# Performance work log

Measured on AMD Instinct MI355X. Metric: run time of the kernel, lower is better.

## Reference

```python
import jax, jax.numpy as jnp
import numpy as np

B, S, D_IN, D_OUT = 4, 2048, 1024, 1024


def setup_inputs() -> dict:
    key = jax.random.key(0)
    ks = jax.random.split(key, 7)
    s_in = 1.0 / np.sqrt(D_IN)
    return {
        "x": jax.random.normal(ks[0], (B, S, D_IN), dtype=jnp.float32),
        "Wq": jax.random.uniform(ks[1], (D_IN, D_OUT), jnp.float32, -s_in, s_in),
        "bq": jax.random.uniform(ks[2], (D_OUT,), jnp.float32, -s_in, s_in),
        "Wk": jax.random.uniform(ks[3], (D_IN, D_OUT), jnp.float32, -s_in, s_in),
        "bk": jax.random.uniform(ks[4], (D_OUT,), jnp.float32, -s_in, s_in),
        "Wv": jax.random.uniform(ks[5], (D_IN, D_OUT), jnp.float32, -s_in, s_in),
        "bv": jax.random.uniform(ks[6], (D_OUT,), jnp.float32, -s_in, s_in),
    }


def reference(x, Wq, bq, Wk, bk, Wv, bv):
    # Linear projections (torch Linear: x @ W^T + b; here W stored as [in,out])
    q = x @ Wq + bq  # [B,S,D]
    k = x @ Wk + bk
    v = x @ Wv + bv
    scores = jnp.einsum("bqd,bkd->bqk", q, k)  # [B,S,S]
    # causal mask: positions j > i masked with -inf (applied BEFORE scaling,
    # which is equivalent since -inf/sqrt(d) == -inf)
    seq = scores.shape[-1]
    causal = jnp.tril(jnp.ones((seq, seq), dtype=bool))
    masked = jnp.where(causal, scores, -jnp.inf)
    attn = jax.nn.softmax(masked / np.sqrt(k.shape[-1]), axis=-1)
    # dropout p=0.0 -> identity
    return attn @ v  # [B,S,D]
```

## Files before the change

kernel.cpp:

```cpp
#include <hip/hip_runtime.h>

typedef unsigned short u16;
typedef unsigned int u32;
typedef __attribute__((ext_vector_type(8))) short short8;
typedef __attribute__((ext_vector_type(4))) float f32x4;

__device__ __forceinline__ u16 f2bf(float f) {
    u32 u = __float_as_uint(f);
    u32 r = (u + 0x7fffu + ((u >> 16) & 1u)) >> 16;
    return (u16)r;
}
__device__ __forceinline__ float bf2f(u16 h) {
    return __uint_as_float(((u32)h) << 16);
}

__device__ __forceinline__ void gld16(u16* lds_dst, const u16* g_src) {
    __builtin_amdgcn_global_load_lds(
        (const __attribute__((address_space(1))) unsigned int*)g_src,
        (__attribute__((address_space(3))) unsigned int*)lds_dst,
        16, 0, 0);
}

__global__ void split_x_k(const float* __restrict__ x, u16* __restrict__ xh,
                          u16* __restrict__ xl) {
    long i = ((long)blockIdx.x * 256 + threadIdx.x) * 4;
    float4 f = *(const float4*)(x + i);
    u16 h0 = f2bf(f.x), h1 = f2bf(f.y), h2 = f2bf(f.z), h3 = f2bf(f.w);
    u16 l0 = f2bf(f.x - bf2f(h0)), l1 = f2bf(f.y - bf2f(h1));
    u16 l2 = f2bf(f.z - bf2f(h2)), l3 = f2bf(f.w - bf2f(h3));
    uint2 hv, lv;
    hv.x = (u32)h0 | ((u32)h1 << 16); hv.y = (u32)h2 | ((u32)h3 << 16);
    lv.x = (u32)l0 | ((u32)l1 << 16); lv.y = (u32)l2 | ((u32)l3 << 16);
    *(uint2*)(xh + i) = hv;
    *(uint2*)(xl + i) = lv;
}

__global__ void splitT_w_k(const float* __restrict__ Wq, const float* __restrict__ Wk,
                           const float* __restrict__ Wv, u16* __restrict__ wth,
                           u16* __restrict__ wtl) {
    __shared__ float tile[32][33];
    int z = blockIdx.z;
    const float* W = (z == 0) ? Wq : (z == 1) ? Wk : Wv;
    int n0 = blockIdx.x * 32, k0 = blockIdx.y * 32;
    int tx = threadIdx.x, ty = threadIdx.y;
#pragma unroll
    for (int r0 = 0; r0 < 4; ++r0) {
        int r = ty + r0 * 8;
        tile[r][tx] = W[(long)(k0 + r) * 1024 + n0 + tx];
    }
    __syncthreads();
    long zoff = (long)z * 1024 * 1024;
#pragma unroll
    for (int r0 = 0; r0 < 4; ++r0) {
        int r = ty + r0 * 8;
        float f = tile[tx][r];
        u16 h = f2bf(f), l = f2bf(f - bf2f(h));
        long idx = zoff + (long)(n0 + r) * 1024 + k0 + tx;
        wth[idx] = h;
        wtl[idx] = l;
    }
}

__global__ void transpose_v_k(const u16* __restrict__ vh, const u16* __restrict__ vl,
                              u16* __restrict__ vth, u16* __restrict__ vtl) {
    __shared__ u16 th[32][33];
    __shared__ u16 tl[32][33];
    int z = blockIdx.z;
    int d0 = blockIdx.x * 32, s0 = blockIdx.y * 32;
    int tx = threadIdx.x, ty = threadIdx.y;
#pragma unroll
    for (int r0 = 0; r0 < 4; ++r0) {
        int r = ty + r0 * 8;
        long idx = ((long)z * 2048 + s0 + r) * 1024 + d0 + tx;
        th[r][tx] = vh[idx];
        tl[r][tx] = vl[idx];
    }
    __syncthreads();
    long zoff = (long)z * 1024 * 2048;
#pragma unroll
    for (int r0 = 0; r0 < 4; ++r0) {
        int r = ty + r0 * 8;
        long idx = zoff + (long)(d0 + r) * 2048 + s0 + tx;
        vth[idx] = th[tx][r];
        vtl[idx] = tl[tx][r];
    }
}

template <int MODE>
__launch_bounds__(256, 2)
__global__ void gemm_k(const u16* __restrict__ Ah, const u16* __restrict__ Al, long sAz,
                       const u16* __restrict__ Bh, const u16* __restrict__ Bl, long sBz,
                       int lda, int ldb, int Ksize,
                       float* __restrict__ outF, long sCz, int ldc,
                       u16* __restrict__ oh0, u16* __restrict__ oh1, u16* __restrict__ oh2,
                       u16* __restrict__ ol0, u16* __restrict__ ol1, u16* __restrict__ ol2,
                       const float* __restrict__ b0, const float* __restrict__ b1,
                       const float* __restrict__ b2) {
    const int bi = blockIdx.x, bj = blockIdx.y, z = blockIdx.z;
    if (MODE == 1 && bj > bi) return;

    int ksteps = Ksize / 32;
    if (MODE == 2) ksteps = min(ksteps, (bi + 1) * 4);

    Ah += (long)z * sAz; Al += (long)z * sAz;
    Bh += (long)z * sBz; Bl += (long)z * sBz;

    __shared__ u16 lds[4 * 4096];
    u16* tAh = lds;
    u16* tAl = lds + 4096;
    u16* tBh = lds + 8192;
    u16* tBl = lds + 12288;

    const int t = threadIdx.x;
    const int lane = t & 63, w = t >> 6;
    const int wr = w >> 1, wc = w & 1;

    f32x4 acc[4][4] = {};

    const int srow = (lane >> 2);
    const int scol = (lane & 3) * 8;
    const long rowA = (long)bi * 128;
    const long rowB = (long)bj * 128;

    for (int ks = 0; ks < ksteps; ++ks) {
        const int k0 = ks * 32;
#pragma unroll
        for (int i = 0; i < 2; ++i) {
            const int chunk = i * 4 + w;
            const int r = chunk * 16 + srow;
            const long aoff = (rowA + r) * (long)lda + k0 + scol;
            const long boff = (rowB + r) * (long)ldb + k0 + scol;
            gld16(tAh + chunk * 512, Ah + aoff);
            gld16(tAl + chunk * 512, Al + aoff);
            gld16(tBh + chunk * 512, Bh + boff);
            gld16(tBl + chunk * 512, Bl + boff);
        }
        __syncthreads();

        short8 afh[4], afl[4], bfh[4], bfl[4];
        const int fr = lane & 15;
        const int koff = (lane >> 4) * 8;
#pragma unroll
        for (int m = 0; m < 4; ++m) {
            int r = wr * 64 + m * 16 + fr;
            afh[m] = *(const short8*)&tAh[r * 32 + koff];
            afl[m] = *(const short8*)&tAl[r * 32 + koff];
        }
#pragma unroll
        for (int n = 0; n < 4; ++n) {
            int r = wc * 64 + n * 16 + fr;
            bfh[n] = *(const short8*)&tBh[r * 32 + koff];
            bfl[n] = *(const short8*)&tBl[r * 32 + koff];
        }
#pragma unroll
        for (int m = 0; m < 4; ++m)
#pragma unroll
            for (int n = 0; n < 4; ++n) {
                acc[m][n] = __builtin_amdgcn_mfma_f32_16x16x32_bf16(afh[m], bfh[n], acc[m][n], 0, 0, 0);
                acc[m][n] = __builtin_amdgcn_mfma_f32_16x16x32_bf16(afh[m], bfl[n], acc[m][n], 0, 0, 0);
                acc[m][n] = __builtin_amdgcn_mfma_f32_16x16x32_bf16(afl[m], bfh[n], acc[m][n], 0, 0, 0);
            }
        __syncthreads();
    }

    const int row0 = bi * 128 + wr * 64 + (lane >> 4) * 4;
    const int col0 = bj * 128 + wc * 64 + (lane & 15);

    if (MODE == 0) {
        const float* bias = (z == 0) ? b0 : (z == 1) ? b1 : b2;
        u16* oh = (z == 0) ? oh0 : (z == 1) ? oh1 : oh2;
        u16* ol = (z == 0) ? ol0 : (z == 1) ? ol1 : ol2;
#pragma unroll
        for (int n = 0; n < 4; ++n) {
            float bv = bias[col0 + n * 16];
#pragma unroll
            for (int m = 0; m < 4; ++m)
#pragma unroll
                for (int j = 0; j < 4; ++j) {
                    float v = acc[m][n][j] + bv;
                    long idx = (long)(row0 + m * 16 + j) * ldc + col0 + n * 16;
                    u16 h = f2bf(v);
                    oh[idx] = h;
                    ol[idx] = f2bf(v - bf2f(h));
                }
        }
    } else {
        float* o = outF + (long)z * sCz;
#pragma unroll
        for (int m = 0; m < 4; ++m)
#pragma unroll
            for (int n = 0; n < 4; ++n)
#pragma unroll
                for (int j = 0; j < 4; ++j)
                    o[(long)(row0 + m * 16 + j) * ldc + col0 + n * 16] = acc[m][n][j];
    }
}

__global__ void softmax_k(const float* __restrict__ S, u16* __restrict__ Ph,
                          u16* __restrict__ Pl) {
    const long row = blockIdx.x;
    const int batch = (int)(row >> 11), i = (int)(row & 2047);
    const float* srow = S + ((long)batch * 2048 + i) * 2048;
    u16* ph = Ph + row * 2048;
    u16* pl = Pl + row * 2048;
    const int t = threadIdx.x;

    float v[8];
    float m = -1e30f;
#pragma unroll
    for (int j = 0; j < 8; ++j) {
        int c = j * 256 + t;
        float x = (c <= i) ? srow[c] : -1e30f;
        v[j] = x;
        m = fmaxf(m, x);
    }
#pragma unroll
    for (int off = 32; off; off >>= 1) m = fmaxf(m, __shfl_xor(m, off));
    __shared__ float redm[4], reds[4];
    if ((t & 63) == 0) redm[t >> 6] = m;
    __syncthreads();
    m = fmaxf(fmaxf(redm[0], redm[1]), fmaxf(redm[2], redm[3]));

    float p[8];
    float s = 0.f;
#pragma unroll
    for (int j = 0; j < 8; ++j) {
        int c = j * 256 + t;
        float e = (c <= i) ? __expf((v[j] - m) * 0.03125f) : 0.f;
        p[j] = e;
        s += e;
    }
#pragma unroll
    for (int off = 32; off; off >>= 1) s += __shfl_xor(s, off);
    if ((t & 63) == 0) reds[t >> 6] = s;
    __syncthreads();
    s = reds[0] + reds[1] + reds[2] + reds[3];
    const float inv = 1.f / s;
#pragma unroll
    for (int j = 0; j < 8; ++j) {
        int c = j * 256 + t;
        float o = p[j] * inv;
        u16 h = f2bf(o);
        ph[c] = h;
        pl[c] = f2bf(o - bf2f(h));
    }
}

extern "C" void kernel_launch(void* const* d_in, const int* in_sizes, int n_in,
                              void* d_out, int out_size, void* d_ws, size_t ws_size,
                              hipStream_t stream) {
    const float* x  = (const float*)d_in[0];
    const float* Wq = (const float*)d_in[1];
    const float* bq = (const float*)d_in[2];
    const float* Wk = (const float*)d_in[3];
    const float* bk = (const float*)d_in[4];
    const float* Wv = (const float*)d_in[5];
    const float* bv = (const float*)d_in[6];
    float* out = (float*)d_out;
    char* ws = (char*)d_ws;
    const size_t MB = 1ull << 20;

    u16* xs_hi = (u16*)(ws + 0 * MB);
    u16* xs_lo = (u16*)(ws + 16 * MB);
    u16* wt_hi = (u16*)(ws + 32 * MB);
    u16* wt_lo = (u16*)(ws + 38 * MB);
    float* S   = (float*)(ws + 0 * MB);
    u16* q_hi = (u16*)(ws + 64 * MB);
    u16* q_lo = (u16*)(ws + 80 * MB);
    u16* k_hi = (u16*)(ws + 96 * MB);
    u16* k_lo = (u16*)(ws + 112 * MB);
    u16* P_hi = (u16*)(ws + 64 * MB);
    u16* P_lo = (u16*)(ws + 96 * MB);
    u16* v_hi  = (u16*)(ws + 128 * MB);
    u16* v_lo  = (u16*)(ws + 144 * MB);
    u16* vt_hi = (u16*)(ws + 160 * MB);
    u16* vt_lo = (u16*)(ws + 176 * MB);

    split_x_k<<<8192, 256, 0, stream>>>(x, xs_hi, xs_lo);
    splitT_w_k<<<dim3(32, 32, 3), dim3(32, 8), 0, stream>>>(Wq, Wk, Wv, wt_hi, wt_lo);
    gemm_k<0><<<dim3(64, 8, 3), 256, 0, stream>>>(
        xs_hi, xs_lo, 0L, wt_hi, wt_lo, 1024L * 1024, 1024, 1024, 1024,
        nullptr, 0L, 1024, q_hi, k_hi, v_hi, q_lo, k_lo, v_lo, bq, bk, bv);
    transpose_v_k<<<dim3(32, 64, 4), dim3(32, 8), 0, stream>>>(v_hi, v_lo, vt_hi, vt_lo);
    gemm_k<1><<<dim3(16, 16, 4), 256, 0, stream>>>(
        q_hi, q_lo, 2048L * 1024, k_hi, k_lo, 2048L * 1024, 1024, 1024, 1024,
        S, 2048L * 2048, 2048, nullptr, nullptr, nullptr, nullptr, nullptr, nullptr,
        nullptr, nullptr, nullptr);
    softmax_k<<<8192, 256, 0, stream>>>(S, P_hi, P_lo);
    gemm_k<2><<<dim3(16, 8, 4), 256, 0, stream>>>(
        P_hi, P_lo, 2048L * 2048, vt_hi, vt_lo, 1024L * 2048, 2048, 2048, 2048,
        out, 2048L * 1024, 1024, nullptr, nullptr, nullptr, nullptr, nullptr, nullptr,
        nullptr, nullptr, nullptr);
}
```

Before: 473.1 us.

## Triple-buffer GEMM LDS loads with swizzle, 512-thread blocks, trim softmax stores

Restructures the split-bf16 GEMM into a 3-slot LDS ring. Global-to-LDS loads for step h+2 are issued while step h computes, using explicit vmcnt waits and a single barrier per step in place of two syncthreads. Blocks go to 512 threads (8 waves), tile width becomes a template parameter (256 columns for the projection GEMM, 128 for the others), LDS accesses get an XOR swizzle to avoid bank conflicts, and MFMA sections run under raised wave priority. Softmax now skips writing P entries beyond the 128-aligned causal limit that the PV GEMM never reads. In exchange, LDS use per block grows and hand-tuned waitcnt counts tie correctness to the exact number of loads issued per stage.

Measured after the change: 468.4 us. No clear change (-1.0%).

```diff
diff --git a/kernel.cpp b/kernel.cpp
--- a/kernel.cpp
+++ b/kernel.cpp
@@ -86,8 +86,8 @@
     }
 }
 
-template <int MODE>
-__launch_bounds__(256, 2)
+template <int MODE, int NF>
+__launch_bounds__(512, 2)
 __global__ void gemm_k(const u16* __restrict__ Ah, const u16* __restrict__ Al, long sAz,
                        const u16* __restrict__ Bh, const u16* __restrict__ Bl, long sBz,
                        int lda, int ldb, int Ksize,
@@ -96,82 +96,103 @@
                        u16* __restrict__ ol0, u16* __restrict__ ol1, u16* __restrict__ ol2,
                        const float* __restrict__ b0, const float* __restrict__ b1,
                        const float* __restrict__ b2) {
+    constexpr int BN = NF * 64;
+    constexpr int SLOT = 8192 + NF * 4096;
+    __shared__ u16 lds[3 * SLOT];
+
     const int bi = blockIdx.x, bj = blockIdx.y, z = blockIdx.z;
     if (MODE == 1 && bj > bi) return;
-
-    int ksteps = Ksize / 32;
-    if (MODE == 2) ksteps = min(ksteps, (bi + 1) * 4);
-
-    Ah += (long)z * sAz; Al += (long)z * sAz;
-    Bh += (long)z * sBz; Bl += (long)z * sBz;
-
-    __shared__ u16 lds[4 * 4096];
-    u16* tAh = lds;
-    u16* tAl = lds + 4096;
-    u16* tBh = lds + 8192;
-    u16* tBl = lds + 12288;
-
-    const int t = threadIdx.x;
-    const int lane = t & 63, w = t >> 6;
-    const int wr = w >> 1, wc = w & 1;
-
-    f32x4 acc[4][4] = {};
-
-    const int srow = (lane >> 2);
-    const int scol = (lane & 3) * 8;
-    const long rowA = (long)bi * 128;
-    const long rowB = (long)bj * 128;
-
-    for (int ks = 0; ks < ksteps; ++ks) {
-        const int k0 = ks * 32;
-#pragma unroll
-        for (int i = 0; i < 2; ++i) {
-            const int chunk = i * 4 + w;
-            const int r = chunk * 16 + srow;
-            const long aoff = (rowA + r) * (long)lda + k0 + scol;
-            const long boff = (rowB + r) * (long)ldb + k0 + scol;
-            gld16(tAh + chunk * 512, Ah + aoff);
-            gld16(tAl + chunk * 512, Al + aoff);
-            gld16(tBh + chunk * 512, Bh + boff);
-            gld16(tBl + chunk * 512, Bl + boff);
-        }
-        __syncthreads();
-
-        short8 afh[4], afl[4], bfh[4], bfl[4];
-        const int fr = lane & 15;
-        const int koff = (lane >> 4) * 8;
+    int nsteps = Ksize / 32;
+    if (MODE == 2) nsteps = min(nsteps, (bi + 1) * 4);
+
+    const u16* gA_h = Ah + (long)z * sAz;
+    const u16* gA_l = Al + (long)z * sAz;
+    const u16* gB_h = Bh + (long)z * sBz;
+    const u16* gB_l = Bl + (long)z * sBz;
+
+    const int tid = threadIdx.x;
+    const int lane = tid & 63, w = tid >> 6;
+    const int wr = w >> 2, wc = w & 3;
+
+    const int srow = tid >> 2;
+    const int ls8 = (((tid & 3) ^ ((tid >> 3) & 3)) << 3);
+    const long aoff  = ((long)bi * 128 + srow) * lda + ls8;
+    const long boff0 = ((long)bj * BN + srow) * ldb + ls8;
+    const long boff1 = boff0 + 128L * (long)ldb;
+    const int wbase = w * 512;
+
+    f32x4 acc[4][NF] = {};
+
+    const int fr = lane & 15;
+    const int ps8 = (((lane >> 4) ^ ((fr >> 1) & 3)) << 3);
+
+    auto stage = [&](int slot, int step) {
+        const int k0 = step * 32;
+        u16* sb = lds + slot * SLOT;
+        gld16(sb + wbase,              gA_h + aoff + k0);
+        gld16(sb + 4096 + wbase,       gA_l + aoff + k0);
+        gld16(sb + 8192 + wbase,       gB_h + boff0 + k0);
+        if constexpr (NF == 4) gld16(sb + 12288 + wbase, gB_h + boff1 + k0);
+        gld16(sb + 8192 + NF * 2048 + wbase, gB_l + boff0 + k0);
+        if constexpr (NF == 4) gld16(sb + 8192 + NF * 2048 + 4096 + wbase, gB_l + boff1 + k0);
+    };
+
+    auto compute = [&](int slot) {
+        const u16* LA = lds + slot * SLOT;
+        const u16* LB = LA + 8192;
+        short8 afh[4], afl[4], bfh[NF], bfl[NF];
 #pragma unroll
         for (int m = 0; m < 4; ++m) {
-            int r = wr * 64 + m * 16 + fr;
-            afh[m] = *(const short8*)&tAh[r * 32 + koff];
-            afl[m] = *(const short8*)&tAl[r * 32 + koff];
-        }
-#pragma unroll
-        for (int n = 0; n < 4; ++n) {
-            int r = wc * 64 + n * 16 + fr;
-            bfh[n] = *(const short8*)&tBh[r * 32 + koff];
-            bfl[n] = *(const short8*)&tBl[r * 32 + koff];
-        }
+            int off = (wr * 64 + m * 16 + fr) * 32 + ps8;
+            afh[m] = *(const short8*)(LA + off);
+            afl[m] = *(const short8*)(LA + 4096 + off);
+        }
+#pragma unroll
+        for (int n = 0; n < NF; ++n) {
+            int off = (wc * (NF * 16) + n * 16 + fr) * 32 + ps8;
+            bfh[n] = *(const short8*)(LB + off);
+            bfl[n] = *(const short8*)(LB + NF * 2048 + off);
+        }
+        __builtin_amdgcn_s_setprio(1);
 #pragma unroll
         for (int m = 0; m < 4; ++m)
 #pragma unroll
-            for (int n = 0; n < 4; ++n) {
+            for (int n = 0; n < NF; ++n) {
                 acc[m][n] = __builtin_amdgcn_mfma_f32_16x16x32_bf16(afh[m], bfh[n], acc[m][n], 0, 0, 0);
                 acc[m][n] = __builtin_amdgcn_mfma_f32_16x16x32_bf16(afh[m], bfl[n], acc[m][n], 0, 0, 0);
                 acc[m][n] = __builtin_amdgcn_mfma_f32_16x16x32_bf16(afl[m], bfh[n], acc[m][n], 0, 0, 0);
             }
-        __syncthreads();
+        __builtin_amdgcn_s_setprio(0);
+    };
+
+    stage(0, 0);
+    if (nsteps > 1) stage(1, 1);
+
+    int cs = 0, ns = 2;
+    for (int h = 0; h < nsteps; ++h) {
+        if (h + 1 < nsteps) {
+            if constexpr (NF == 4) asm volatile("s_waitcnt vmcnt(6)" ::: "memory");
+            else                   asm volatile("s_waitcnt vmcnt(4)" ::: "memory");
+        } else {
+            asm volatile("s_waitcnt vmcnt(0)" ::: "memory");
+        }
+        __builtin_amdgcn_s_barrier();
+        __builtin_amdgcn_sched_barrier(0);
+        if (h + 2 < nsteps) stage(ns, h + 2);
+        compute(cs);
+        cs = (cs == 2) ? 0 : cs + 1;
+        ns = (ns == 2) ? 0 : ns + 1;
     }
 
     const int row0 = bi * 128 + wr * 64 + (lane >> 4) * 4;
-    const int col0 = bj * 128 + wc * 64 + (lane & 15);
+    const int col0 = bj * BN + wc * (NF * 16) + (lane & 15);
 
     if (MODE == 0) {
         const float* bias = (z == 0) ? b0 : (z == 1) ? b1 : b2;
         u16* oh = (z == 0) ? oh0 : (z == 1) ? oh1 : oh2;
         u16* ol = (z == 0) ? ol0 : (z == 1) ? ol1 : ol2;
 #pragma unroll
-        for (int n = 0; n < 4; ++n) {
+        for (int n = 0; n < NF; ++n) {
             float bv = bias[col0 + n * 16];
 #pragma unroll
             for (int m = 0; m < 4; ++m)
@@ -189,7 +210,7 @@
 #pragma unroll
         for (int m = 0; m < 4; ++m)
 #pragma unroll
-            for (int n = 0; n < 4; ++n)
+            for (int n = 0; n < NF; ++n)
 #pragma unroll
                 for (int j = 0; j < 4; ++j)
                     o[(long)(row0 + m * 16 + j) * ldc + col0 + n * 16] = acc[m][n][j];
@@ -199,11 +220,12 @@
 __global__ void softmax_k(const float* __restrict__ S, u16* __restrict__ Ph,
                           u16* __restrict__ Pl) {
     const long row = blockIdx.x;
-    const int batch = (int)(row >> 11), i = (int)(row & 2047);
-    const float* srow = S + ((long)batch * 2048 + i) * 2048;
+    const int i = (int)(row & 2047);
+    const float* srow = S + row * 2048;
     u16* ph = Ph + row * 2048;
     u16* pl = Pl + row * 2048;
     const int t = threadIdx.x;
+    const int limit = ((i >> 7) + 1) << 7;
 
     float v[8];
     float m = -1e30f;
@@ -239,10 +261,12 @@
 #pragma unroll
     for (int j = 0; j < 8; ++j) {
         int c = j * 256 + t;
-        float o = p[j] * inv;
-        u16 h = f2bf(o);
-        ph[c] = h;
-        pl[c] = f2bf(o - bf2f(h));
+        if (c < limit) {
+            float o = p[j] * inv;
+            u16 h = f2bf(o);
+            ph[c] = h;
+            pl[c] = f2bf(o - bf2f(h));
+        }
     }
 }
 
@@ -278,16 +302,16 @@
 
     split_x_k<<<8192, 256, 0, stream>>>(x, xs_hi, xs_lo);
     splitT_w_k<<<dim3(32, 32, 3), dim3(32, 8), 0, stream>>>(Wq, Wk, Wv, wt_hi, wt_lo);
-    gemm_k<0><<<dim3(64, 8, 3), 256, 0, stream>>>(
+    gemm_k<0, 4><<<dim3(64, 4, 3), 512, 0, stream>>>(
         xs_hi, xs_lo, 0L, wt_hi, wt_lo, 1024L * 1024, 1024, 1024, 1024,
         nullptr, 0L, 1024, q_hi, k_hi, v_hi, q_lo, k_lo, v_lo, bq, bk, bv);
     transpose_v_k<<<dim3(32, 64, 4), dim3(32, 8), 0, stream>>>(v_hi, v_lo, vt_hi, vt_lo);
-    gemm_k<1><<<dim3(16, 16, 4), 256, 0, stream>>>(
+    gemm_k<1, 2><<<dim3(16, 16, 4), 512, 0, stream>>>(
         q_hi, q_lo, 2048L * 1024, k_hi, k_lo, 2048L * 1024, 1024, 1024, 1024,
         S, 2048L * 2048, 2048, nullptr, nullptr, nullptr, nullptr, nullptr, nullptr,
         nullptr, nullptr, nullptr);
     softmax_k<<<8192, 256, 0, stream>>>(S, P_hi, P_lo);
-    gemm_k<2><<<dim3(16, 8, 4), 256, 0, stream>>>(
+    gemm_k<2, 2><<<dim3(16, 8, 4), 512, 0, stream>>>(
         P_hi, P_lo, 2048L * 2048, vt_hi, vt_lo, 1024L * 2048, 2048, 2048, 2048,
         out, 2048L * 1024, 1024, nullptr, nullptr, nullptr, nullptr, nullptr, nullptr,
         nullptr, nullptr, nullptr);
```
